# Kernel tuning notes

Measured on AMD Instinct MI355X. Metric: run time of the kernel, lower is better.

Reference implementation:

```python
import jax, jax.numpy as jnp
import numpy as np

V, E, H, B, P, Q = 100000, 300, 256, 64, 400, 50
NEG = -1e7


def _gru_param(k, s=0.08):
    k1, k2, k3, k4 = jax.random.split(k, 4)
    return (jax.random.normal(k1, (2, 3 * H, E)) * s,
            jax.random.normal(k2, (2, 3 * H, H)) * s,
            jax.random.normal(k3, (2, 3 * H)) * s,
            jax.random.normal(k4, (2, 3 * H)) * s)


def setup_inputs() -> dict:
    key = jax.random.key(0)
    ks = jax.random.split(key, 10)
    emb = (jax.random.normal(ks[0], (V, E)) * 0.1).at[0].set(0.0)  # padding_idx=0 row zeroed
    passage = jax.random.randint(ks[1], (B, P), 1, V)
    question = jax.random.randint(ks[2], (B, Q), 1, V)
    # variable lengths, padding (token 0) at the tail like pack_padded_sequence assumes
    p_len = 200 + (jnp.arange(B) * 7) % (P - 200)
    q_len = 20 + (jnp.arange(B) * 3) % (Q - 20)
    passage = jnp.where(jnp.arange(P)[None, :] < p_len[:, None], passage, 0)
    question = jnp.where(jnp.arange(Q)[None, :] < q_len[:, None], question, 0)
    pW_ih, pW_hh, pb_ih, pb_hh = _gru_param(ks[3])
    qW_ih, qW_hh, qb_ih, qb_hh = _gru_param(ks[4])
    start_w = jax.random.normal(ks[5], (6 * H,)) * 0.05
    start_b = jax.random.normal(ks[6], ()) * 0.05
    end_w = jax.random.normal(ks[7], (6 * H,)) * 0.05
    end_b = jax.random.normal(ks[8], ()) * 0.05
    return dict(passage=passage, question=question, emb=emb,
                pW_ih=pW_ih, pW_hh=pW_hh, pb_ih=pb_ih, pb_hh=pb_hh,
                qW_ih=qW_ih, qW_hh=qW_hh, qb_ih=qb_ih, qb_hh=qb_hh,
                start_w=start_w, start_b=start_b, end_w=end_w, end_b=end_b)


def bi_gru(x, mask, Wih, Whh, bih, bhh):
    """Bidirectional GRU with packed-sequence-equivalent masking.
    x: (B,T,E), mask: (B,T) float. Returns (B,T,2H). Padded outputs are 0,
    and the backward pass starts at the true last token (mask freezes state)."""
    m = mask[..., None]                                          # (B,T,1)
    xproj = jnp.einsum('bte,dhe->dbth', x, Wih) + bih[:, None, None, :]  # (2,B,T,3H)

    def run(xp, mm, Whh_d, bhh_d):
        def step(h, inp):
            xt, mt = inp                                         # (B,3H),(B,1)
            hp = h @ Whh_d.T + bhh_d
            r = jax.nn.sigmoid(xt[:, :H] + hp[:, :H])
            z = jax.nn.sigmoid(xt[:, H:2 * H] + hp[:, H:2 * H])
            n = jnp.tanh(xt[:, 2 * H:] + r * hp[:, 2 * H:])
            h_new = (1 - z) * n + z * h
            h_new = mt * h_new + (1 - mt) * h
            return h_new, h_new * mt
        h0 = jnp.zeros((xp.shape[0], H), xp.dtype)
        _, out = jax.lax.scan(step, h0, (xp.transpose(1, 0, 2), mm.transpose(1, 0, 2)))
        return out.transpose(1, 0, 2)                            # (B,T,H)

    fwd = run(xproj[0], m, Whh[0], bhh[0])
    bwd = run(xproj[1][:, ::-1], m[:, ::-1], Whh[1], bhh[1])[:, ::-1]
    return jnp.concatenate([fwd, bwd], axis=-1)


def reference(passage, question, emb,
              pW_ih, pW_hh, pb_ih, pb_hh,
              qW_ih, qW_hh, qb_ih, qb_hh,
              start_w, start_b, end_w, end_b):
    p_mask = (passage != 0).astype(jnp.float32)                  # (B,P)
    q_mask = (question != 0).astype(jnp.float32)                 # (B,Q)
    Hp = bi_gru(emb[passage], p_mask, pW_ih, pW_hh, pb_ih, pb_hh)  # (B,P,2H)
    Hq = bi_gru(emb[question], q_mask, qW_ih, qW_hh, qb_ih, qb_hh)  # (B,Q,2H)

    # Trilinear attention: decompose Linear over the cat([p, q, p*q]) terms
    w1, w2, w3 = start_w[:2 * H], start_w[2 * H:4 * H], start_w[4 * H:]
    scores = (Hp @ w1)[:, :, None] + (Hq @ w2)[:, None, :] \
        + jnp.einsum('bpd,bqd->bpq', Hp * w3, Hq) + start_b      # (B,P,Q)

    # allennlp masked_softmax: softmax(vector*mask) * mask, renormalized
    a = jax.nn.softmax(scores * q_mask[:, None, :], axis=-1) * q_mask[:, None, :]
    a = a / (a.sum(axis=-1, keepdims=True) + 1e-13)

    wavg = jnp.einsum('bpq,bqd->bpd', a, Hq)                     # (B,P,2H)
    combined = jnp.concatenate([Hp, wavg, Hp * wavg], axis=-1)   # (B,P,6H)

    start_logits = jnp.where(p_mask > 0, combined @ start_w + start_b, NEG)
    end_logits = jnp.where(p_mask > 0, combined @ end_w + end_b, NEG)
    log_mask = jnp.log(p_mask + 1e-45)
    softmax_start = jax.nn.log_softmax(start_logits + log_mask, axis=-1)
    softmax_end = jax.nn.log_softmax(end_logits + log_mask, axis=-1)
    return start_logits, end_logits, softmax_start, softmax_end
```

## Files before the change

kernel.cpp:

```cpp
#include <hip/hip_runtime.h>
#include <math.h>

constexpr int Bb = 64;
constexpr int Pp = 400;
constexpr int Qq = 50;
constexpr int Ee = 300;
constexpr int Hh = 256;
constexpr int H3 = 768;
constexpr int Dd = 512;

#define NEGC (-10000000.0f)
#define LOGTINY (-103.278929903f)

typedef _Float16 h2 __attribute__((ext_vector_type(2)));
typedef _Float16 f16x8 __attribute__((ext_vector_type(8)));
typedef float f32x4 __attribute__((ext_vector_type(4)));

__device__ __forceinline__ float allred(float v){
  #pragma unroll
  for (int off = 1; off < 64; off <<= 1) v += __shfl_xor(v, off);
  return v;
}
__device__ __forceinline__ float allmax(float v){
  #pragma unroll
  for (int off = 1; off < 64; off <<= 1) v = fmaxf(v, __shfl_xor(v, off));
  return v;
}
__device__ __forceinline__ float sigm(float x){ return 1.f / (1.f + expf(-x)); }

__device__ __forceinline__ float dot2f(unsigned a, unsigned b, float c){
#if __has_builtin(__builtin_amdgcn_fdot2)
  return __builtin_amdgcn_fdot2(__builtin_bit_cast(h2, a), __builtin_bit_cast(h2, b), c, false);
#else
  float r = c;
  asm("v_dot2_f32_f16 %0, %1, %2, %0" : "+v"(r) : "v"(a), "v"(b));
  return r;
#endif
}

#define U4C(v,c) ((c)==0?(v).x:((c)==1?(v).y:((c)==2?(v).z:(v).w)))

__global__ __launch_bounds__(256) void prep_emb16(const float* __restrict__ emb,
                                                  _Float16* __restrict__ emb16){
  size_t idx = (size_t)blockIdx.x * 256 + threadIdx.x;
  if (idx >= (size_t)100000 * 160) return;
  int col2 = (int)(idx % 160);
  size_t row = idx / 160;
  int c = col2 * 2;
  float2 v = make_float2(0.f, 0.f);
  if (c < Ee) v = *(const float2*)(emb + row * Ee + c);
  h2 o = { (_Float16)v.x, (_Float16)v.y };
  *(h2*)(emb16 + row * 320 + c) = o;
}

__global__ __launch_bounds__(256) void prep_wih16(const float* __restrict__ pW,
                                                  const float* __restrict__ qW,
                                                  _Float16* __restrict__ wih16){
  int idx = blockIdx.x * 256 + threadIdx.x;
  if (idx >= 2 * 2 * 768 * 160) return;
  int col2 = idx % 160;
  int r = idx / 160;
  int g = r / 1536;
  int dh = r % 1536;
  int c = col2 * 2;
  const float* W = g ? qW : pW;
  float2 v = make_float2(0.f, 0.f);
  if (c < Ee) v = *(const float2*)(W + (size_t)dh * Ee + c);
  h2 o = { (_Float16)v.x, (_Float16)v.y };
  *(h2*)(wih16 + (size_t)r * 320 + c) = o;
}

__global__ __launch_bounds__(256) void prep_w16(const float* __restrict__ pW,
                                                const float* __restrict__ qW,
                                                unsigned* __restrict__ w16){
  int idx = blockIdx.x * 256 + threadIdx.x;
  if (idx >= 2 * 2 * 3 * 16 * 512 * 4) return;
  int c = idx & 3;
  int t = (idx >> 2) & 511;
  int q = (idx >> 11) & 15;
  int gg = idx >> 15;
  int gate = gg % 3, gd = gg / 3;
  int d = gd & 1, g = gd >> 1;
  int j = t & 255, half = t >> 8;
  int p = half * 64 + q * 4 + c;
  int row = gate * 256 + j;
  const float* W = g ? qW : pW;
  const float* src = W + ((size_t)d * H3 + row) * Hh + 2 * p;
  _Float16 a = (_Float16)src[0], b = (_Float16)src[1];
  unsigned short ua, ub;
  __builtin_memcpy(&ua, &a, 2); __builtin_memcpy(&ub, &b, 2);
  unsigned val = (unsigned)ua | ((unsigned)ub << 16);

  size_t u4idx;
  if (q < 4)       u4idx = ((size_t)gg * 4 + q) * 512 + t;
  else if (q < 10) u4idx = 24576 + ((size_t)gg * 6 + (q - 4)) * 512 + t;
  else             u4idx = 61440 + ((size_t)gg * 6 + (q - 10)) * 512 + t;
  w16[u4idx * 4 + c] = val;
}

__global__ __launch_bounds__(512) void xproj_mfma(const int* __restrict__ tok,
                                                  const _Float16* __restrict__ emb16,
                                                  const _Float16* __restrict__ wih16,
                                                  const float* __restrict__ bih,
                                                  _Float16* __restrict__ xp, int T){
  __shared__ __align__(16) _Float16 Af[128][72];
  __shared__ __align__(16) _Float16 Bf[128][72];
  int tid = threadIdx.x;
  int m0 = blockIdx.y * 128;
  int nt = blockIdx.x;
  int d = nt / 6, h0 = (nt % 6) * 128;
  int wid = tid >> 6, lane = tid & 63;
  int wr = wid >> 2, wc = wid & 3;

  int r0 = tid >> 3;
  int r1 = (tid + 512) >> 3;
  int cc = (tid & 7) * 8;
  const _Float16* eA0 = emb16 + (size_t)tok[m0 + r0] * 320;
  const _Float16* eA1 = emb16 + (size_t)tok[m0 + r1] * 320;
  const _Float16* wB0 = wih16 + ((size_t)d * H3 + h0 + r0) * 320;
  const _Float16* wB1 = wih16 + ((size_t)d * H3 + h0 + r1) * 320;

  f32x4 acc[4][2] = {};

  for (int k0 = 0; k0 < 320; k0 += 64){
    *(f16x8*)&Af[r0][cc] = *(const f16x8*)(eA0 + k0 + cc);
    *(f16x8*)&Af[r1][cc] = *(const f16x8*)(eA1 + k0 + cc);
    *(f16x8*)&Bf[r0][cc] = *(const f16x8*)(wB0 + k0 + cc);
    *(f16x8*)&Bf[r1][cc] = *(const f16x8*)(wB1 + k0 + cc);
    __syncthreads();
    #pragma unroll
    for (int kc = 0; kc < 2; ++kc){
      int kb = kc * 32 + (lane >> 4) * 8;
      f16x8 af[4], bf[2];
      #pragma unroll
      for (int i = 0; i < 4; ++i) af[i] = *(const f16x8*)&Af[wr * 64 + i * 16 + (lane & 15)][kb];
      #pragma unroll
      for (int jn = 0; jn < 2; ++jn) bf[jn] = *(const f16x8*)&Bf[wc * 32 + jn * 16 + (lane & 15)][kb];
      #pragma unroll
      for (int i = 0; i < 4; ++i)
        #pragma unroll
        for (int jn = 0; jn < 2; ++jn)
          acc[i][jn] = __builtin_amdgcn_mfma_f32_16x16x32_f16(af[i], bf[jn], acc[i][jn], 0, 0, 0);
    }
    __syncthreads();
  }

  #pragma unroll
  for (int jn = 0; jn < 2; ++jn){
    int h = h0 + wc * 32 + jn * 16 + (lane & 15);
    float bv = bih[d * H3 + h];
    #pragma unroll
    for (int i = 0; i < 4; ++i){
      #pragma unroll
      for (int r = 0; r < 4; ++r){
        int m = m0 + wr * 64 + i * 16 + (lane >> 4) * 4 + r;
        int bI = m / T, tI = m - bI * T;
        xp[(((size_t)d * Bb + bI) * T + tI) * H3 + h] = (_Float16)(acc[i][jn][r] + bv);
      }
    }
  }
}

__global__ __launch_bounds__(512)
void gru_kernel(const int* __restrict__ ptok,
                const int* __restrict__ qtok,
                const _Float16* __restrict__ xpp,
                const _Float16* __restrict__ xpq,
                const unsigned* __restrict__ w16,
                const float* __restrict__ pbhh,
                const float* __restrict__ qbhh,
                float* __restrict__ Hp,
                float* __restrict__ Hq){
  int wg = blockIdx.x;
  bool isp = wg < 128;
  int lw = isp ? wg : wg - 128;
  int d = lw & 1, b = lw >> 1;
  int T = isp ? Pp : Qq;
  const int* tok = (isp ? ptok : qtok) + b * T;
  const _Float16* xrow = (isp ? xpp : xpq) + ((size_t)d * Bb + b) * T * H3;
  int gd = (isp ? 0 : 2) + d;
  const float* bhh = (isp ? pbhh : qbhh) + d * H3;
  float* Hout = (isp ? Hp : Hq) + (size_t)b * T * Dd + d * Hh;

  __shared__ __align__(16) uint4 ldsW[18 * 512];
  __shared__ unsigned hbuf[2][128];
  __shared__ float pa[Hh], pb[Hh], pn[Hh];

  int t = threadIdx.x;
  int j = t & 255, half = t >> 8, lane = t & 63;

  const uint4* wR = (const uint4*)w16 + (size_t)(gd * 3) * 4 * 512;
  unsigned wr0[16], wr1[16], wr2[16];
  #pragma unroll
  for (int q = 0; q < 4; ++q){
    uint4 v0 = wR[(0 * 4 + q) * 512 + t];
    uint4 v1 = wR[(1 * 4 + q) * 512 + t];
    uint4 v2 = wR[(2 * 4 + q) * 512 + t];
    wr0[4 * q + 0] = v0.x; wr0[4 * q + 1] = v0.y; wr0[4 * q + 2] = v0.z; wr0[4 * q + 3] = v0.w;
    wr1[4 * q + 0] = v1.x; wr1[4 * q + 1] = v1.y; wr1[4 * q + 2] = v1.z; wr1[4 * q + 3] = v1.w;
    wr2[4 * q + 0] = v2.x; wr2[4 * q + 1] = v2.y; wr2[4 * q + 2] = v2.z; wr2[4 * q + 3] = v2.w;
  }
  #pragma unroll
  for (int i = 0; i < 16; ++i){
    asm volatile("" : "+v"(wr0[i]));
    asm volatile("" : "+v"(wr1[i]));
    asm volatile("" : "+v"(wr2[i]));
  }
  const uint4* wL = (const uint4*)w16 + 24576 + (size_t)(gd * 3) * 6 * 512;
  #pragma unroll
  for (int u = 0; u < 18; ++u) ldsW[u * 512 + t] = wL[u * 512 + t];
  const uint4* wS = (const uint4*)w16 + 61440 + (size_t)(gd * 3) * 6 * 512;

  float bh0 = bhh[j], bh1 = bhh[Hh + j], bh2 = bhh[2 * Hh + j];
  float h_old = 0.f;
  if (t < 128) hbuf[1][t] = 0u;
  __syncthreads();

  int t0 = d ? (T - 1) : 0;
  float pre0 = 0.f, pre1 = 0.f, pre2 = 0.f;
  if (half == 0){
    pre0 = (float)xrow[(size_t)t0 * H3 + j];
    pre1 = (float)xrow[(size_t)t0 * H3 + Hh + j];
    pre2 = (float)xrow[(size_t)t0 * H3 + 2 * Hh + j];
  }

  for (int s = 0; s < T; ++s){
    int tt = d ? (T - 1 - s) : s;
    unsigned vh = hbuf[(s + 1) & 1][half * 64 + lane];
    float a0 = 0.f, a1 = 0.f, a2 = 0.f;

    uint4 sA0 = wS[0 * 512 + t], sA1 = wS[1 * 512 + t], sA2 = wS[2 * 512 + t],
          sA3 = wS[3 * 512 + t], sA4 = wS[4 * 512 + t], sA5 = wS[5 * 512 + t];
    uint4 sB0 = wS[6 * 512 + t],  sB1 = wS[7 * 512 + t],  sB2 = wS[8 * 512 + t],
          sB3 = wS[9 * 512 + t],  sB4 = wS[10 * 512 + t], sB5 = wS[11 * 512 + t];

    #pragma unroll
    for (int q = 0; q < 4; ++q)
      #pragma unroll
      for (int c = 0; c < 4; ++c){
        unsigned hv = (unsigned)__builtin_amdgcn_readlane((int)vh, q * 4 + c);
        a0 = dot2f(wr0[4 * q + c], hv, a0);
        a1 = dot2f(wr1[4 * q + c], hv, a1);
        a2 = dot2f(wr2[4 * q + c], hv, a2);
      }

    uint4 sC0 = wS[12 * 512 + t], sC1 = wS[13 * 512 + t], sC2 = wS[14 * 512 + t],
          sC3 = wS[15 * 512 + t], sC4 = wS[16 * 512 + t], sC5 = wS[17 * 512 + t];

    #pragma unroll
    for (int qb = 0; qb < 6; ++qb){
      uint4 l0 = ldsW[(0 * 6 + qb) * 512 + t];
      uint4 l1 = ldsW[(1 * 6 + qb) * 512 + t];
      uint4 l2 = ldsW[(2 * 6 + qb) * 512 + t];
      #pragma unroll
      for (int c = 0; c < 4; ++c){
        unsigned hv = (unsigned)__builtin_amdgcn_readlane((int)vh, 16 + qb * 4 + c);
        a0 = dot2f(U4C(l0, c), hv, a0);
        a1 = dot2f(U4C(l1, c), hv, a1);
        a2 = dot2f(U4C(l2, c), hv, a2);
      }
    }

    #define CONS(v, qi, ACC) { _Pragma("unroll") \
      for (int c = 0; c < 4; ++c){ \
        unsigned hv = (unsigned)__builtin_amdgcn_readlane((int)vh, 40 + (qi) * 4 + c); \
        ACC = dot2f(U4C(v, c), hv, ACC); } }
    CONS(sA0, 0, a0) CONS(sA1, 1, a0) CONS(sA2, 2, a0)
    CONS(sA3, 3, a0) CONS(sA4, 4, a0) CONS(sA5, 5, a0)
    CONS(sB0, 0, a1) CONS(sB1, 1, a1) CONS(sB2, 2, a1)
    CONS(sB3, 3, a1) CONS(sB4, 4, a1) CONS(sB5, 5, a1)
    CONS(sC0, 0, a2) CONS(sC1, 1, a2) CONS(sC2, 2, a2)
    CONS(sC3, 3, a2) CONS(sC4, 4, a2) CONS(sC5, 5, a2)
    #undef CONS

    if (half == 1){ pa[j] = a0; pb[j] = a1; pn[j] = a2; }
    __syncthreads();
    if (half == 0){
      float xt0 = pre0, xt1 = pre1, xt2 = pre2;
      if (s + 1 < T){
        int tn = d ? (T - 2 - s) : (s + 1);
        pre0 = (float)xrow[(size_t)tn * H3 + j];
        pre1 = (float)xrow[(size_t)tn * H3 + Hh + j];
        pre2 = (float)xrow[(size_t)tn * H3 + 2 * Hh + j];
      }
      float g0 = a0 + pa[j] + bh0;
      float g1 = a1 + pb[j] + bh1;
      float g2 = a2 + pn[j] + bh2;
      float r = sigm(xt0 + g0);
      float z = sigm(xt1 + g1);
      float n = tanhf(xt2 + r * g2);
      float hnew = (1.f - z) * n + z * h_old;
      float m = (tok[tt] != 0) ? 1.f : 0.f;
      float hm = m * hnew + (1.f - m) * h_old;
      h_old = hm;
      ((_Float16*)hbuf[s & 1])[j] = (_Float16)hm;
      Hout[(size_t)tt * Dd + j] = hm * m;
    }
    __syncthreads();
  }
}

__global__ __launch_bounds__(512) void attn_kernel(const float* __restrict__ Hp,
                                                   const float* __restrict__ Hq,
                                                   const int* __restrict__ ptok,
                                                   const int* __restrict__ qtok,
                                                   const float* __restrict__ start_w,
                                                   const float* __restrict__ sbp,
                                                   const float* __restrict__ end_w,
                                                   const float* __restrict__ ebp,
                                                   float* __restrict__ out){
  extern __shared__ __align__(16) float lds[];
  float* hqs = lds;
  float* s2s = hqs + Qq * Dd;
  float* qms = s2s + 64;
  float* scw = qms + 64;
  float* aw  = scw + 512;

  int b = blockIdx.y, pc = blockIdx.x;
  int tid = threadIdx.x, wid = tid >> 6, lane = tid & 63;
  float sb = sbp[0], eb = ebp[0];

  float w1r[8], w2r[8], w3r[8], e1r[8], e2r[8], e3r[8];
  #pragma unroll
  for (int i = 0; i < 8; ++i){
    int c = lane * 8 + i;
    w1r[i] = start_w[c]; w2r[i] = start_w[Dd + c]; w3r[i] = start_w[2 * Dd + c];
    e1r[i] = end_w[c];   e2r[i] = end_w[Dd + c];   e3r[i] = end_w[2 * Dd + c];
  }
  for (int idx = tid; idx < Qq * Dd; idx += 512) hqs[idx] = Hq[(size_t)b * Qq * Dd + idx];
  __syncthreads();

  for (int q = wid; q < Qq; q += 8){
    float part = 0.f;
    const float* hq = hqs + q * Dd + lane * 8;
    #pragma unroll
    for (int i = 0; i < 8; ++i) part += hq[i] * w2r[i];
    part = allred(part);
    if (lane == 0){
      s2s[q] = part;
      qms[q] = (qtok[b * Qq + q] != 0) ? 1.f : 0.f;
    }
  }
  __syncthreads();

  for (int p = pc * 100 + wid; p < pc * 100 + 100; p += 8){
    const float* hprow = Hp + ((size_t)b * Pp + p) * Dd + lane * 8;
    float4 hv0 = *(const float4*)hprow;
    float4 hv1 = *(const float4*)(hprow + 4);
    float hpc[8] = {hv0.x, hv0.y, hv0.z, hv0.w, hv1.x, hv1.y, hv1.z, hv1.w};
    float hw3[8], he3[8];
    float s1 = 0.f, ed = 0.f;
    #pragma unroll
    for (int i = 0; i < 8; ++i){
      hw3[i] = hpc[i] * w3r[i];
      he3[i] = hpc[i] * e3r[i];
      s1 += hpc[i] * w1r[i];
      ed += hpc[i] * e1r[i];
    }
    #pragma unroll
    for (int off = 1; off < 64; off <<= 1){
      s1 += __shfl_xor(s1, off);
      ed += __shfl_xor(ed, off);
    }
    for (int q = 0; q < Qq; ++q){
      const float4* hq4 = (const float4*)(hqs + q * Dd + lane * 8);
      float4 a0 = hq4[0], a1 = hq4[1];
      float dot = hw3[0] * a0.x + hw3[1] * a0.y + hw3[2] * a0.z + hw3[3] * a0.w
                + hw3[4] * a1.x + hw3[5] * a1.y + hw3[6] * a1.z + hw3[7] * a1.w;
      dot = allred(dot);
      if (lane == 0) scw[wid * 64 + q] = (s1 + s2s[q] + dot + sb) * qms[q];
    }
    float v = (lane < Qq) ? scw[wid * 64 + lane] : -1e30f;
    float M = allmax(v);
    float ev = (lane < Qq) ? expf(v - M) : 0.f;
    float S = allred(ev);
    float am = (lane < Qq) ? (ev / S) * qms[lane] : 0.f;
    float Sm = allred(am);
    float af = am / (Sm + 1e-13f);
    if (lane < Qq) aw[wid * 64 + lane] = af;
    float wv[8] = {0.f, 0.f, 0.f, 0.f, 0.f, 0.f, 0.f, 0.f};
    for (int q = 0; q < Qq; ++q){
      float aq = aw[wid * 64 + q];
      const float4* hq4 = (const float4*)(hqs + q * Dd + lane * 8);
      float4 a0 = hq4[0], a1 = hq4[1];
      wv[0] += aq * a0.x; wv[1] += aq * a0.y; wv[2] += aq * a0.z; wv[3] += aq * a0.w;
      wv[4] += aq * a1.x; wv[5] += aq * a1.y; wv[6] += aq * a1.z; wv[7] += aq * a1.w;
    }
    float acc2 = 0.f, acc3 = 0.f, acc4 = 0.f, acc5 = 0.f;
    #pragma unroll
    for (int i = 0; i < 8; ++i){
      acc2 += wv[i] * w2r[i];
      acc3 += hw3[i] * wv[i];
      acc4 += wv[i] * e2r[i];
      acc5 += he3[i] * wv[i];
    }
    #pragma unroll
    for (int off = 1; off < 64; off <<= 1){
      acc2 += __shfl_xor(acc2, off);
      acc3 += __shfl_xor(acc3, off);
      acc4 += __shfl_xor(acc4, off);
      acc5 += __shfl_xor(acc5, off);
    }
    if (lane == 0){
      bool pm = (ptok[b * Pp + p] != 0);
      out[(size_t)b * Pp + p]                   = pm ? (s1 + acc2 + acc3 + sb) : NEGC;
      out[(size_t)Bb * Pp + (size_t)b * Pp + p] = pm ? (ed + acc4 + acc5 + eb) : NEGC;
    }
  }
}

__global__ __launch_bounds__(512) void lsm_kernel(const int* __restrict__ ptok,
                                                  float* __restrict__ out){
  int b = blockIdx.x >> 1, sel = blockIdx.x & 1;
  const float* lg = out + (size_t)sel * Bb * Pp + (size_t)b * Pp;
  float* o = out + (size_t)(2 + sel) * Bb * Pp + (size_t)b * Pp;
  int tid = threadIdx.x;
  __shared__ float red1[8];
  __shared__ float red2[8];
  float x = -1e30f;
  if (tid < Pp) x = lg[tid] + ((ptok[b * Pp + tid] != 0) ? 0.f : LOGTINY);
  float m = allmax(x);
  if ((tid & 63) == 0) red1[tid >> 6] = m;
  __syncthreads();
  float M = red1[0];
  #pragma unroll
  for (int i = 1; i < 8; ++i) M = fmaxf(M, red1[i]);
  float e = (tid < Pp) ? expf(x - M) : 0.f;
  float s = allred(e);
  if ((tid & 63) == 0) red2[tid >> 6] = s;
  __syncthreads();
  float S = 0.f;
  #pragma unroll
  for (int i = 0; i < 8; ++i) S += red2[i];
  if (tid < Pp) o[tid] = (x - M) - logf(S);
}

extern "C" void kernel_launch(void* const* d_in, const int* in_sizes, int n_in,
                              void* d_out, int out_size, void* d_ws, size_t ws_size,
                              hipStream_t stream){
  const int*   passage  = (const int*)d_in[0];
  const int*   question = (const int*)d_in[1];
  const float* emb      = (const float*)d_in[2];
  const float* pW_ih    = (const float*)d_in[3];
  const float* pW_hh    = (const float*)d_in[4];
  const float* pb_ih    = (const float*)d_in[5];
  const float* pb_hh    = (const float*)d_in[6];
  const float* qW_ih    = (const float*)d_in[7];
  const float* qW_hh    = (const float*)d_in[8];
  const float* qb_ih    = (const float*)d_in[9];
  const float* qb_hh    = (const float*)d_in[10];
  const float* start_w  = (const float*)d_in[11];
  const float* start_b  = (const float*)d_in[12];
  const float* end_w    = (const float*)d_in[13];
  const float* end_b    = (const float*)d_in[14];
  float* out = (float*)d_out;

  float*     ws    = (float*)d_ws;
  unsigned*  w16   = (unsigned*)ws;
  _Float16*  emb16 = (_Float16*)(ws + 393216);
  _Float16*  wih16 = (_Float16*)(ws + 16393216);
  _Float16*  xpp   = (_Float16*)(ws + 16884736);
  _Float16*  xpq   = (_Float16*)(ws + 36545536);
  float*     Hp    = ws + 39003136;
  float*     Hq    = ws + 52110336;

  hipLaunchKernelGGL(prep_w16, dim3(1536), dim3(256), 0, stream, pW_hh, qW_hh, w16);
  hipLaunchKernelGGL(prep_emb16, dim3(62500), dim3(256), 0, stream, emb, emb16);
  hipLaunchKernelGGL(prep_wih16, dim3(1920), dim3(256), 0, stream, pW_ih, qW_ih, wih16);
  hipLaunchKernelGGL(xproj_mfma, dim3(12, 200), dim3(512), 0, stream,
                     passage, emb16, wih16, pb_ih, xpp, Pp);
  hipLaunchKernelGGL(xproj_mfma, dim3(12, 25), dim3(512), 0, stream,
                     question, emb16, wih16 + (size_t)2 * H3 * 320, qb_ih, xpq, Qq);
  hipLaunchKernelGGL(gru_kernel, dim3(256), dim3(512), 0, stream,
                     passage, question, xpp, xpq, w16, pb_hh, qb_hh, Hp, Hq);
  size_t attn_lds = (size_t)(Qq * Dd + 64 + 64 + 512 + 512) * sizeof(float);
  hipLaunchKernelGGL(attn_kernel, dim3(4, 64), dim3(512), attn_lds, stream,
                     Hp, Hq, passage, question, start_w, start_b, end_w, end_b, out);
  hipLaunchKernelGGL(lsm_kernel, dim3(128), dim3(512), 0, stream, passage, out);
}
```

Baseline: 964.3 us.

## Gather only used embedding rows to fp16 and rebalance GRU weight residency

Replaces the full-vocabulary embedding fp16 conversion with a gather that converts only the token rows referenced by passage and question into dense per-row buffers, which xproj then reads directly. It also changes the split of recurrent weights in the GRU kernel: more chunks are held in registers, the same number in LDS, and fewer are streamed from global memory. The streamed loads are now interleaved per gate with the LDS work to hide latency. The aim is to cut the large prep conversion traffic and the per-step global weight loads, at the cost of more register pressure in the GRU kernel.

Result: no change. 964.9 us (+0.1%).

```diff
diff --git a/kernel.cpp b/kernel.cpp
--- a/kernel.cpp
+++ b/kernel.cpp
@@ -40,17 +40,24 @@
 
 #define U4C(v,c) ((c)==0?(v).x:((c)==1?(v).y:((c)==2?(v).z:(v).w)))
 
-__global__ __launch_bounds__(256) void prep_emb16(const float* __restrict__ emb,
-                                                  _Float16* __restrict__ emb16){
-  size_t idx = (size_t)blockIdx.x * 256 + threadIdx.x;
-  if (idx >= (size_t)100000 * 160) return;
-  int col2 = (int)(idx % 160);
-  size_t row = idx / 160;
-  int c = col2 * 2;
-  float2 v = make_float2(0.f, 0.f);
-  if (c < Ee) v = *(const float2*)(emb + row * Ee + c);
-  h2 o = { (_Float16)v.x, (_Float16)v.y };
-  *(h2*)(emb16 + row * 320 + c) = o;
+__global__ __launch_bounds__(256) void gather_a(const int* __restrict__ ptok,
+                                                const int* __restrict__ qtok,
+                                                const float* __restrict__ emb,
+                                                _Float16* __restrict__ Agp,
+                                                _Float16* __restrict__ Agq){
+  int idx = blockIdx.x * 256 + threadIdx.x;
+  if (idx >= (25600 + 3200) * 40) return;
+  int ck = idx % 40;
+  int row = idx / 40;
+  int tokv; _Float16* dst;
+  if (row < 25600){ tokv = ptok[row]; dst = Agp + (size_t)row * 320; }
+  else { int r = row - 25600; tokv = qtok[r]; dst = Agq + (size_t)r * 320; }
+  int c = ck * 8;
+  const float* src = emb + (size_t)tokv * Ee;
+  f16x8 v;
+  #pragma unroll
+  for (int i = 0; i < 8; ++i) v[i] = (c + i < Ee) ? (_Float16)src[c + i] : (_Float16)0.f;
+  *(f16x8*)(dst + c) = v;
 }
 
 __global__ __launch_bounds__(256) void prep_wih16(const float* __restrict__ pW,
@@ -92,14 +99,13 @@
   unsigned val = (unsigned)ua | ((unsigned)ub << 16);
 
   size_t u4idx;
-  if (q < 4)       u4idx = ((size_t)gg * 4 + q) * 512 + t;
-  else if (q < 10) u4idx = 24576 + ((size_t)gg * 6 + (q - 4)) * 512 + t;
-  else             u4idx = 61440 + ((size_t)gg * 6 + (q - 10)) * 512 + t;
+  if (q < 5)       u4idx = ((size_t)gg * 5 + q) * 512 + t;
+  else if (q < 11) u4idx = 30720 + ((size_t)gg * 6 + (q - 5)) * 512 + t;
+  else             u4idx = 67584 + ((size_t)gg * 5 + (q - 11)) * 512 + t;
   w16[u4idx * 4 + c] = val;
 }
 
-__global__ __launch_bounds__(512) void xproj_mfma(const int* __restrict__ tok,
-                                                  const _Float16* __restrict__ emb16,
+__global__ __launch_bounds__(512) void xproj_mfma(const _Float16* __restrict__ Ag,
                                                   const _Float16* __restrict__ wih16,
                                                   const float* __restrict__ bih,
                                                   _Float16* __restrict__ xp, int T){
@@ -115,8 +121,8 @@
   int r0 = tid >> 3;
   int r1 = (tid + 512) >> 3;
   int cc = (tid & 7) * 8;
-  const _Float16* eA0 = emb16 + (size_t)tok[m0 + r0] * 320;
-  const _Float16* eA1 = emb16 + (size_t)tok[m0 + r1] * 320;
+  const _Float16* eA0 = Ag + (size_t)(m0 + r0) * 320;
+  const _Float16* eA1 = Ag + (size_t)(m0 + r1) * 320;
   const _Float16* wB0 = wih16 + ((size_t)d * H3 + h0 + r0) * 320;
   const _Float16* wB1 = wih16 + ((size_t)d * H3 + h0 + r1) * 320;
 
@@ -188,28 +194,29 @@
 
   int t = threadIdx.x;
   int j = t & 255, half = t >> 8, lane = t & 63;
-
-  const uint4* wR = (const uint4*)w16 + (size_t)(gd * 3) * 4 * 512;
-  unsigned wr0[16], wr1[16], wr2[16];
-  #pragma unroll
-  for (int q = 0; q < 4; ++q){
-    uint4 v0 = wR[(0 * 4 + q) * 512 + t];
-    uint4 v1 = wR[(1 * 4 + q) * 512 + t];
-    uint4 v2 = wR[(2 * 4 + q) * 512 + t];
+  const uint4* u4w = (const uint4*)w16;
+
+  unsigned wr0[20], wr1[20], wr2[20];
+  #pragma unroll
+  for (int q = 0; q < 5; ++q){
+    uint4 v0 = u4w[((size_t)(gd * 3 + 0) * 5 + q) * 512 + t];
+    uint4 v1 = u4w[((size_t)(gd * 3 + 1) * 5 + q) * 512 + t];
+    uint4 v2 = u4w[((size_t)(gd * 3 + 2) * 5 + q) * 512 + t];
     wr0[4 * q + 0] = v0.x; wr0[4 * q + 1] = v0.y; wr0[4 * q + 2] = v0.z; wr0[4 * q + 3] = v0.w;
     wr1[4 * q + 0] = v1.x; wr1[4 * q + 1] = v1.y; wr1[4 * q + 2] = v1.z; wr1[4 * q + 3] = v1.w;
     wr2[4 * q + 0] = v2.x; wr2[4 * q + 1] = v2.y; wr2[4 * q + 2] = v2.z; wr2[4 * q + 3] = v2.w;
   }
   #pragma unroll
-  for (int i = 0; i < 16; ++i){
+  for (int i = 0; i < 20; ++i){
     asm volatile("" : "+v"(wr0[i]));
     asm volatile("" : "+v"(wr1[i]));
     asm volatile("" : "+v"(wr2[i]));
   }
-  const uint4* wL = (const uint4*)w16 + 24576 + (size_t)(gd * 3) * 6 * 512;
-  #pragma unroll
-  for (int u = 0; u < 18; ++u) ldsW[u * 512 + t] = wL[u * 512 + t];
-  const uint4* wS = (const uint4*)w16 + 61440 + (size_t)(gd * 3) * 6 * 512;
+
+  #pragma unroll
+  for (int u = 0; u < 18; ++u)
+    ldsW[u * 512 + t] = u4w[30720 + ((size_t)gd * 18 + u) * 512 + t];
+  const uint4* wS = u4w + 67584 + (size_t)(gd * 3) * 5 * 512;
 
   float bh0 = bhh[j], bh1 = bhh[Hh + j], bh2 = bhh[2 * Hh + j];
   float h_old = 0.f;
@@ -229,49 +236,50 @@
     unsigned vh = hbuf[(s + 1) & 1][half * 64 + lane];
     float a0 = 0.f, a1 = 0.f, a2 = 0.f;
 
-    uint4 sA0 = wS[0 * 512 + t], sA1 = wS[1 * 512 + t], sA2 = wS[2 * 512 + t],
-          sA3 = wS[3 * 512 + t], sA4 = wS[4 * 512 + t], sA5 = wS[5 * 512 + t];
-    uint4 sB0 = wS[6 * 512 + t],  sB1 = wS[7 * 512 + t],  sB2 = wS[8 * 512 + t],
-          sB3 = wS[9 * 512 + t],  sB4 = wS[10 * 512 + t], sB5 = wS[11 * 512 + t];
-
-    #pragma unroll
-    for (int q = 0; q < 4; ++q)
+    #define LPH(ql) { \
+      uint4 l0 = ldsW[(0 * 6 + (ql)) * 512 + t]; \
+      uint4 l1 = ldsW[(1 * 6 + (ql)) * 512 + t]; \
+      uint4 l2 = ldsW[(2 * 6 + (ql)) * 512 + t]; \
+      _Pragma("unroll") \
+      for (int c = 0; c < 4; ++c){ \
+        unsigned hv = (unsigned)__builtin_amdgcn_readlane((int)vh, 20 + (ql) * 4 + c); \
+        a0 = dot2f(U4C(l0, c), hv, a0); \
+        a1 = dot2f(U4C(l1, c), hv, a1); \
+        a2 = dot2f(U4C(l2, c), hv, a2); } }
+    #define SCQ(ACC, si, A) { _Pragma("unroll") \
+      for (int c = 0; c < 4; ++c){ \
+        unsigned hv = (unsigned)__builtin_amdgcn_readlane((int)vh, 44 + (si) * 4 + c); \
+        ACC = dot2f(U4C(A, c), hv, ACC); } }
+    #define SISSG(g, A0, A1, A2, A3, A4) \
+      uint4 A0 = wS[((g) * 5 + 0) * 512 + t]; \
+      uint4 A1 = wS[((g) * 5 + 1) * 512 + t]; \
+      uint4 A2 = wS[((g) * 5 + 2) * 512 + t]; \
+      uint4 A3 = wS[((g) * 5 + 3) * 512 + t]; \
+      uint4 A4 = wS[((g) * 5 + 4) * 512 + t];
+
+    SISSG(0, s00, s01, s02, s03, s04)
+
+    #pragma unroll
+    for (int q = 0; q < 5; ++q)
       #pragma unroll
       for (int c = 0; c < 4; ++c){
-        unsigned hv = (unsigned)__builtin_amdgcn_readlane((int)vh, q * 4 + c);
-        a0 = dot2f(wr0[4 * q + c], hv, a0);
-        a1 = dot2f(wr1[4 * q + c], hv, a1);
-        a2 = dot2f(wr2[4 * q + c], hv, a2);
+        unsigned hv = (unsigned)__builtin_amdgcn_readlane((int)vh, 4 * q + c);
+        a0 = dot2f(wr0[q * 4 + c], hv, a0);
+        a1 = dot2f(wr1[q * 4 + c], hv, a1);
+        a2 = dot2f(wr2[q * 4 + c], hv, a2);
       }
 
-    uint4 sC0 = wS[12 * 512 + t], sC1 = wS[13 * 512 + t], sC2 = wS[14 * 512 + t],
-          sC3 = wS[15 * 512 + t], sC4 = wS[16 * 512 + t], sC5 = wS[17 * 512 + t];
-
-    #pragma unroll
-    for (int qb = 0; qb < 6; ++qb){
-      uint4 l0 = ldsW[(0 * 6 + qb) * 512 + t];
-      uint4 l1 = ldsW[(1 * 6 + qb) * 512 + t];
-      uint4 l2 = ldsW[(2 * 6 + qb) * 512 + t];
-      #pragma unroll
-      for (int c = 0; c < 4; ++c){
-        unsigned hv = (unsigned)__builtin_amdgcn_readlane((int)vh, 16 + qb * 4 + c);
-        a0 = dot2f(U4C(l0, c), hv, a0);
-        a1 = dot2f(U4C(l1, c), hv, a1);
-        a2 = dot2f(U4C(l2, c), hv, a2);
-      }
-    }
-
-    #define CONS(v, qi, ACC) { _Pragma("unroll") \
-      for (int c = 0; c < 4; ++c){ \
-        unsigned hv = (unsigned)__builtin_amdgcn_readlane((int)vh, 40 + (qi) * 4 + c); \
-        ACC = dot2f(U4C(v, c), hv, ACC); } }
-    CONS(sA0, 0, a0) CONS(sA1, 1, a0) CONS(sA2, 2, a0)
-    CONS(sA3, 3, a0) CONS(sA4, 4, a0) CONS(sA5, 5, a0)
-    CONS(sB0, 0, a1) CONS(sB1, 1, a1) CONS(sB2, 2, a1)
-    CONS(sB3, 3, a1) CONS(sB4, 4, a1) CONS(sB5, 5, a1)
-    CONS(sC0, 0, a2) CONS(sC1, 1, a2) CONS(sC2, 2, a2)
-    CONS(sC3, 3, a2) CONS(sC4, 4, a2) CONS(sC5, 5, a2)
-    #undef CONS
+    LPH(0) LPH(1)
+    SCQ(a0, 0, s00) SCQ(a0, 1, s01) SCQ(a0, 2, s02) SCQ(a0, 3, s03) SCQ(a0, 4, s04)
+    SISSG(1, s10, s11, s12, s13, s14)
+    LPH(2) LPH(3)
+    SCQ(a1, 0, s10) SCQ(a1, 1, s11) SCQ(a1, 2, s12) SCQ(a1, 3, s13) SCQ(a1, 4, s14)
+    SISSG(2, s20, s21, s22, s23, s24)
+    LPH(4) LPH(5)
+    SCQ(a2, 0, s20) SCQ(a2, 1, s21) SCQ(a2, 2, s22) SCQ(a2, 3, s23) SCQ(a2, 4, s24)
+    #undef LPH
+    #undef SCQ
+    #undef SISSG
 
     if (half == 1){ pa[j] = a0; pb[j] = a1; pn[j] = a2; }
     __syncthreads();
@@ -457,20 +465,22 @@
 
   float*     ws    = (float*)d_ws;
   unsigned*  w16   = (unsigned*)ws;
-  _Float16*  emb16 = (_Float16*)(ws + 393216);
-  _Float16*  wih16 = (_Float16*)(ws + 16393216);
-  _Float16*  xpp   = (_Float16*)(ws + 16884736);
-  _Float16*  xpq   = (_Float16*)(ws + 36545536);
-  float*     Hp    = ws + 39003136;
-  float*     Hq    = ws + 52110336;
+  _Float16*  wih16 = (_Float16*)(ws + 393216);
+  _Float16*  Agp   = (_Float16*)(ws + 884736);
+  _Float16*  Agq   = (_Float16*)(ws + 4980736);
+  _Float16*  xpp   = (_Float16*)(ws + 5492736);
+  _Float16*  xpq   = (_Float16*)(ws + 25153536);
+  float*     Hp    = ws + 27611136;
+  float*     Hq    = ws + 40718336;
 
   hipLaunchKernelGGL(prep_w16, dim3(1536), dim3(256), 0, stream, pW_hh, qW_hh, w16);
-  hipLaunchKernelGGL(prep_emb16, dim3(62500), dim3(256), 0, stream, emb, emb16);
+  hipLaunchKernelGGL(gather_a, dim3(4500), dim3(256), 0, stream,
+                     passage, question, emb, Agp, Agq);
   hipLaunchKernelGGL(prep_wih16, dim3(1920), dim3(256), 0, stream, pW_ih, qW_ih, wih16);
   hipLaunchKernelGGL(xproj_mfma, dim3(12, 200), dim3(512), 0, stream,
-                     passage, emb16, wih16, pb_ih, xpp, Pp);
+                     Agp, wih16, pb_ih, xpp, Pp);
   hipLaunchKernelGGL(xproj_mfma, dim3(12, 25), dim3(512), 0, stream,
-                     question, emb16, wih16 + (size_t)2 * H3 * 320, qb_ih, xpq, Qq);
+                     Agq, wih16 + (size_t)2 * H3 * 320, qb_ih, xpq, Qq);
   hipLaunchKernelGGL(gru_kernel, dim3(256), dim3(512), 0, stream,
                      passage, question, xpp, xpq, w16, pb_hh, qb_hh, Hp, Hq);
   size_t attn_lds = (size_t)(Qq * Dd + 64 + 64 + 512 + 512) * sizeof(float);
```
